# Kernel optimization log

Measured on AMD Instinct MI355X. Metric: run time of the kernel, lower is better.

The kernel has to match this reference:

```python
import jax, jax.numpy as jnp
import numpy as np

B, C, T = 8, 512, 2048
G = 32          # GroupNorm groups
HEADS = 8       # C // head_channels(64)
EPS = 1e-5


def setup_inputs() -> dict:
    key = jax.random.key(0)
    ks = jax.random.split(key, 7)
    s = 0.02
    return {
        "x": jax.random.normal(ks[0], (B, C, T), dtype=jnp.float32),
        "gn_w": jnp.ones((C,), dtype=jnp.float32),
        "gn_b": jnp.zeros((C,), dtype=jnp.float32),
        "qkv_w": jax.random.normal(ks[1], (3 * C, C), dtype=jnp.float32) * s,
        "qkv_b": jnp.zeros((3 * C,), dtype=jnp.float32),
        "proj_w": jax.random.normal(ks[2], (C, C), dtype=jnp.float32) * s,
        "proj_b": jnp.zeros((C,), dtype=jnp.float32),
    }


def reference(x, gn_w, gn_b, qkv_w, qkv_b, proj_w, proj_b):
    b, c, t = x.shape
    ch = c // HEADS
    # GroupNorm(32, C): normalize over (channels-in-group, T)
    xg = x.reshape(b, G, (c // G) * t)
    mu = jnp.mean(xg, axis=-1, keepdims=True)
    var = jnp.var(xg, axis=-1, keepdims=True)
    h = ((xg - mu) * jax.lax.rsqrt(var + EPS)).reshape(b, c, t)
    h = h * gn_w[:, None] + gn_b[:, None]
    # 1x1 Conv1d -> pointwise linear over channels
    qkv = jnp.einsum('oc,bct->bot', qkv_w, h) + qkv_b[:, None]  # [b, 3c, t]
    q, k, v = jnp.split(qkv, 3, axis=1)
    scale = ch ** -0.25
    q = (q * scale).reshape(b * HEADS, ch, t)
    k = (k * scale).reshape(b * HEADS, ch, t)
    v = v.reshape(b * HEADS, ch, t)
    w = jnp.einsum('bct,bcs->bts', q, k)  # [b*H, t, t]
    w = jax.nn.softmax(w.astype(jnp.float32), axis=-1).astype(q.dtype)
    a = jnp.einsum('bts,bcs->bct', w, v).reshape(b, c, t)
    out = jnp.einsum('oc,bct->bot', proj_w, a) + proj_b[:, None]
    return x + out
```

## Files before the change

### kernel.cpp

```cpp
#include <hip/hip_runtime.h>
#include <hip/hip_bf16.h>
#include <math.h>

#define NB 8
#define NC 512
#define NT 2048
#define NG 32
#define NH 8
#define CH 64

typedef __attribute__((ext_vector_type(8))) short short8;
typedef __attribute__((ext_vector_type(4))) short short4v;
typedef __attribute__((ext_vector_type(4))) float floatx4;
typedef __attribute__((ext_vector_type(2))) unsigned int uintx2;
typedef __attribute__((ext_vector_type(4))) unsigned int uintx4;

static __device__ __forceinline__ short f2bf(float f) {
    __hip_bfloat16 h = __float2bfloat16(f);
    return *reinterpret_cast<short*>(&h);
}

static __device__ __forceinline__ int pk2bf_trunc(float lo, float hi) {
    return (int)__builtin_amdgcn_perm(__builtin_bit_cast(unsigned, hi),
                                      __builtin_bit_cast(unsigned, lo),
                                      0x07060302u);
}

static __device__ __forceinline__ void gload_lds16(const short* g, short* l) {
    __builtin_amdgcn_global_load_lds(
        (const __attribute__((address_space(1))) void*)g,
        (__attribute__((address_space(3))) void*)l, 16, 0, 0);
}

__global__ __launch_bounds__(256) void castw_kernel(
    const float* __restrict__ qw, const float* __restrict__ pw,
    short* __restrict__ qo, short* __restrict__ po)
{
    const int i = blockIdx.x * 256 + threadIdx.x;
    const bool isq = i < 196608;
    const int j = isq ? i : i - 196608;
    float4 v = isq ? ((const float4*)qw)[j] : ((const float4*)pw)[j];
    short4v s;
    s.x = f2bf(v.x); s.y = f2bf(v.y); s.z = f2bf(v.z); s.w = f2bf(v.w);
    if (isq) *(short4v*)&qo[j * 4] = s;
    else     *(short4v*)&po[j * 4] = s;
}

__global__ __launch_bounds__(256) void gn_fused_kernel(
    const float* __restrict__ x, const float* __restrict__ gw,
    const float* __restrict__ gb, short* __restrict__ ht)
{
    __shared__ float xs[16 * NT];
    __shared__ float red[16];
    const int tid = threadIdx.x;
    const int wv = tid >> 6, lane = tid & 63;
    const int f = blockIdx.x;
    const int b = f & 7, g = f >> 3;

    const float* src = x + ((size_t)b * NC + g * 16) * NT;

    #pragma unroll
    for (int i = 0; i < 32; ++i) {
        const int slot = i * 256 + tid;
        gload_lds16((const short*)src + (size_t)slot * 8,
                    (short*)&xs[(i * 256 + wv * 64) * 4]);
    }
    __syncthreads();

    float s = 0.f, ss = 0.f;
    #pragma unroll
    for (int i = 0; i < 32; ++i) {
        float4 v = ((const float4*)xs)[i * 256 + tid];
        s  += v.x + v.y + v.z + v.w;
        ss += v.x*v.x + v.y*v.y + v.z*v.z + v.w*v.w;
    }
    #pragma unroll
    for (int o = 32; o > 0; o >>= 1) {
        s  += __shfl_down(s,  o, 64);
        ss += __shfl_down(ss, o, 64);
    }
    if (lane == 0) { red[wv] = s; red[8 + wv] = ss; }
    __syncthreads();
    const float inv  = 1.f / 32768.f;
    const float mean = (red[0] + red[1] + red[2] + red[3]) * inv;
    const float var  = (red[8] + red[9] + red[10] + red[11]) * inv - mean * mean;
    const float rstd = rsqrtf(var + 1e-5f);

    float wc[16], bc[16];
    #pragma unroll
    for (int ch = 0; ch < 16; ++ch) {
        const float w = gw[g * 16 + ch] * rstd;
        wc[ch] = w;
        bc[ch] = gb[g * 16 + ch] - mean * w;
    }

    #pragma unroll
    for (int k = 0; k < 2; ++k) {
        const int q = k * 256 + tid;
        float4 col[16];
        #pragma unroll
        for (int ch = 0; ch < 16; ++ch)
            col[ch] = *(const float4*)&xs[ch * NT + q * 4];
        short* dst = ht + ((size_t)b * NT + q * 4) * NC + g * 16;
        #pragma unroll
        for (int j = 0; j < 4; ++j) {
            short v16[16];
            #pragma unroll
            for (int ch = 0; ch < 16; ++ch) {
                const float xv = (j == 0) ? col[ch].x : (j == 1) ? col[ch].y
                               : (j == 2) ? col[ch].z : col[ch].w;
                v16[ch] = f2bf(xv * wc[ch] + bc[ch]);
            }
            *(short8*)&dst[(size_t)j * NC]     = *(const short8*)&v16[0];
            *(short8*)&dst[(size_t)j * NC + 8] = *(const short8*)&v16[8];
        }
    }
}

#define BK 32
__global__ __launch_bounds__(256) void qkv_gemm_kernel(
    const short* __restrict__ wb, const short* __restrict__ ht,
    const float* __restrict__ bias,
    short* __restrict__ q_t, short* __restrict__ k_t, short* __restrict__ vv)
{
    __shared__ short As[128 * BK];
    __shared__ short Bs[128 * BK];
    const int tid = threadIdx.x;
    const int wv = tid >> 6, lane = tid & 63;
    const int l16 = lane & 15, quad = lane >> 4;
    const int fblk = blockIdx.y * 128 + blockIdx.x;
    const int jx = fblk >> 3, xcd = fblk & 7;
    const int n0 = (xcd * 16 + jx / 12) * 128;
    const int m0 = (jx % 12) * 128;
    const int wm = wv & 1, wn = wv >> 1;

    floatx4 acc[4][4];
    #pragma unroll
    for (int i = 0; i < 4; ++i)
        #pragma unroll
        for (int j = 0; j < 4; ++j) acc[i][j] = (floatx4){0.f, 0.f, 0.f, 0.f};

    const short* gsrc = (wv < 2) ? wb : ht;
    const int rbase = (wv & 1) * 64;
    const int tile0 = (wv < 2) ? m0 : n0;
    short* lbuf = (wv < 2) ? As : Bs;
    const int lrow = lane >> 2;
    const int lcol = (lane & 3) * 8;

    for (int k0 = 0; k0 < 512; k0 += BK) {
        __syncthreads();
        #pragma unroll
        for (int ch = 0; ch < 4; ++ch) {
            const int row = rbase + ch * 16 + lrow;
            gload_lds16(gsrc + (size_t)(tile0 + row) * 512 + k0 + lcol,
                        lbuf + (rbase + ch * 16) * BK);
        }
        __syncthreads();

        short8 af[4], bfr[4];
        #pragma unroll
        for (int i = 0; i < 4; ++i) {
            af[i]  = *(const short8*)&As[(wm * 64 + i * 16 + l16) * BK + quad * 8];
            bfr[i] = *(const short8*)&Bs[(wn * 64 + i * 16 + l16) * BK + quad * 8];
        }
        #pragma unroll
        for (int i = 0; i < 4; ++i)
            #pragma unroll
            for (int j = 0; j < 4; ++j)
                acc[i][j] = __builtin_amdgcn_mfma_f32_16x16x32_bf16(
                    af[i], bfr[j], acc[i][j], 0, 0, 0);
    }

    const float kscale = 0.35355339059327373f;
    const float qscale = 0.35355339059327373f * 1.4426950408889634f;
    #pragma unroll
    for (int i = 0; i < 4; ++i) {
        const int o16 = m0 + wm * 64 + i * 16;
        const int sel = o16 >> 9;
        const int hh  = (o16 >> 6) & 7;
        const int c16 = o16 & 63;
        const float4 b4 = *(const float4*)&bias[o16 + quad * 4];
        const float sc = (sel == 0) ? qscale : kscale;
        #pragma unroll
        for (int j = 0; j < 4; ++j) {
            const int tg = n0 + wn * 64 + j * 16 + l16;
            const int b = tg >> 11, t = tg & 2047;
            floatx4 v = acc[i][j];
            v[0] += b4.x; v[1] += b4.y; v[2] += b4.z; v[3] += b4.w;
            if (sel < 2) {
                short4v s;
                s.x = f2bf(v[0] * sc); s.y = f2bf(v[1] * sc);
                s.z = f2bf(v[2] * sc); s.w = f2bf(v[3] * sc);
                short* dst = (sel == 0 ? q_t : k_t) +
                    (((size_t)(b * NH + hh) * NT + t) * CH + c16 + quad * 4);
                *(short4v*)dst = s;
            } else {
                short* dst = vv + ((size_t)(b * NH + hh) * CH + c16 + quad * 4) * NT + t;
                #pragma unroll
                for (int r = 0; r < 4; ++r) dst[(size_t)r * NT] = f2bf(v[r]);
            }
        }
    }
}

__global__ __launch_bounds__(512, 4) void attn_kernel(
    const short* __restrict__ qg, const short* __restrict__ kg,
    const short* __restrict__ vg, short* __restrict__ at)
{
    __shared__ short kt[2][64 * 64];
    __shared__ short vs[2][64 * 64];

    const int tid = threadIdx.x;
    const int wv = tid >> 6, lane = tid & 63;
    const int l16 = lane & 15, quad = lane >> 4;
    const int xr = l16 & 7;
    const int f = blockIdx.y * 8 + blockIdx.x;
    const int t0 = (f >> 6) * 256;
    const int bh = ((f >> 3) & 7) * 8 + (f & 7);
    const int b = bh >> 3, hd = bh & 7;
    const short* qh = qg + (size_t)bh * NT * CH;
    const short* kh = kg + (size_t)bh * NT * CH;
    const short* vh = vg + (size_t)bh * CH * NT;

    {
        const int row = tid >> 3, cc = (tid & 7) ^ (row & 7);
        gload_lds16(kh + (size_t)row * CH + cc * 8, &kt[0][wv * 512]);
        gload_lds16(vh + (size_t)row * NT + cc * 8, &vs[0][wv * 512]);
    }

    short8 bq[2][2];
    #pragma unroll
    for (int qt = 0; qt < 2; ++qt) {
        const int row = t0 + wv * 32 + qt * 16 + l16;
        #pragma unroll
        for (int ks = 0; ks < 2; ++ks)
            bq[qt][ks] = *(const short8*)&qh[(size_t)row * CH + ks * 32 + quad * 8];
    }
    __syncthreads();

    floatx4 Oa[4][2];
    #pragma unroll
    for (int ct = 0; ct < 4; ++ct)
        #pragma unroll
        for (int qt = 0; qt < 2; ++qt) Oa[ct][qt] = (floatx4){0.f, 0.f, 0.f, 0.f};
    float l_part[2] = {0.f, 0.f};

    for (int it = 0; it < NT / 64; ++it) {
        __syncthreads();
        if (it + 1 < NT / 64) {
            const int s0n = (it + 1) * 64;
            const int row = tid >> 3, cc = (tid & 7) ^ (row & 7);
            gload_lds16(kh + (size_t)(s0n + row) * CH + cc * 8,
                        &kt[(it + 1) & 1][wv * 512]);
            gload_lds16(vh + (size_t)row * NT + s0n + cc * 8,
                        &vs[(it + 1) & 1][wv * 512]);
        }
        const short* kc = kt[it & 1];
        const short* vc = vs[it & 1];

        floatx4 sacc[4][2];
        #pragma unroll
        for (int nt = 0; nt < 4; ++nt)
            #pragma unroll
            for (int qt = 0; qt < 2; ++qt) sacc[nt][qt] = (floatx4){0.f, 0.f, 0.f, 0.f};
        __builtin_amdgcn_s_setprio(1);
        #pragma unroll
        for (int ks = 0; ks < 2; ++ks) {
            const int c = (quad | (ks << 2)) ^ xr;
            #pragma unroll
            for (int nt = 0; nt < 4; ++nt) {
                short8 ak = *(const short8*)&kc[(nt * 16 + l16) * 64 + c * 8];
                #pragma unroll
                for (int qt = 0; qt < 2; ++qt)
                    sacc[nt][qt] = __builtin_amdgcn_mfma_f32_16x16x32_bf16(
                        ak, bq[qt][ks], sacc[nt][qt], 0, 0, 0);
            }
        }
        __builtin_amdgcn_s_setprio(0);

        unsigned pk01[2][4], pk23[2][4];
        #pragma unroll
        for (int qt = 0; qt < 2; ++qt) {
            float sn[4];
            #pragma unroll
            for (int nt = 0; nt < 4; ++nt) {
                const float p0 = __builtin_amdgcn_exp2f(sacc[nt][qt][0]);
                const float p1 = __builtin_amdgcn_exp2f(sacc[nt][qt][1]);
                const float p2 = __builtin_amdgcn_exp2f(sacc[nt][qt][2]);
                const float p3 = __builtin_amdgcn_exp2f(sacc[nt][qt][3]);
                sn[nt] = (p0 + p1) + (p2 + p3);
                pk01[qt][nt] = (unsigned)pk2bf_trunc(p0, p1);
                pk23[qt][nt] = (unsigned)pk2bf_trunc(p2, p3);
            }
            l_part[qt] += (sn[0] + sn[1]) + (sn[2] + sn[3]);
        }

        #pragma unroll
        for (int ks = 0; ks < 2; ++ks) {
            short8 bp[2];
            #pragma unroll
            for (int qt = 0; qt < 2; ++qt) {
                uintx2 a = __builtin_amdgcn_permlane32_swap(
                    pk01[qt][2 * ks], pk01[qt][2 * ks + 1], false, false);
                uintx2 w02 = __builtin_amdgcn_permlane16_swap(a.x, a.y, false, false);
                uintx2 c2 = __builtin_amdgcn_permlane32_swap(
                    pk23[qt][2 * ks], pk23[qt][2 * ks + 1], false, false);
                uintx2 w13 = __builtin_amdgcn_permlane16_swap(c2.x, c2.y, false, false);
                uintx4 wi = (uintx4){w02.x, w13.x, w02.y, w13.y};
                bp[qt] = __builtin_bit_cast(short8, wi);
            }
            const int c = (quad | (ks << 2)) ^ xr;
            __builtin_amdgcn_s_setprio(1);
            #pragma unroll
            for (int ct = 0; ct < 4; ++ct) {
                short8 av = *(const short8*)&vc[(ct * 16 + l16) * 64 + c * 8];
                #pragma unroll
                for (int qt = 0; qt < 2; ++qt)
                    Oa[ct][qt] = __builtin_amdgcn_mfma_f32_16x16x32_bf16(
                        av, bp[qt], Oa[ct][qt], 0, 0, 0);
            }
            __builtin_amdgcn_s_setprio(0);
        }
    }

    #pragma unroll
    for (int qt = 0; qt < 2; ++qt) {
        float l = l_part[qt];
        l += __shfl_xor(l, 16, 64);
        l += __shfl_xor(l, 32, 64);
        const float rl = 1.f / l;
        const int t = t0 + wv * 32 + qt * 16 + l16;
        short* dst = at + ((size_t)b * NT + t) * NC + hd * CH;
        #pragma unroll
        for (int ct = 0; ct < 4; ++ct) {
            int2 s;
            s.x = pk2bf_trunc(Oa[ct][qt][0] * rl, Oa[ct][qt][1] * rl);
            s.y = pk2bf_trunc(Oa[ct][qt][2] * rl, Oa[ct][qt][3] * rl);
            *(int2*)&dst[ct * 16 + quad * 4] = s;
        }
    }
}

__global__ __launch_bounds__(256) void proj_gemm_kernel(
    const short* __restrict__ wb, const short* __restrict__ at,
    const float* __restrict__ bias, const float* __restrict__ xres,
    float* __restrict__ out)
{
    __shared__ short As[128 * BK];
    __shared__ short Bs[128 * BK];
    const int tid = threadIdx.x;
    const int wv = tid >> 6, lane = tid & 63;
    const int l16 = lane & 15, quad = lane >> 4;
    const int fblk = blockIdx.y * 128 + blockIdx.x;
    const int jx = fblk >> 3, xcd = fblk & 7;
    const int n0 = (xcd * 16 + (jx >> 2)) * 128;
    const int m0 = (jx & 3) * 128;
    const int wm = wv & 1, wn = wv >> 1;

    floatx4 acc[4][4];
    #pragma unroll
    for (int i = 0; i < 4; ++i)
        #pragma unroll
        for (int j = 0; j < 4; ++j) acc[i][j] = (floatx4){0.f, 0.f, 0.f, 0.f};

    const short* gsrc = (wv < 2) ? wb : at;
    const int rbase = (wv & 1) * 64;
    const int tile0 = (wv < 2) ? m0 : n0;
    short* lbuf = (wv < 2) ? As : Bs;
    const int lrow = lane >> 2;
    const int lcol = (lane & 3) * 8;

    for (int k0 = 0; k0 < 512; k0 += BK) {
        __syncthreads();
        #pragma unroll
        for (int ch = 0; ch < 4; ++ch) {
            const int row = rbase + ch * 16 + lrow;
            gload_lds16(gsrc + (size_t)(tile0 + row) * 512 + k0 + lcol,
                        lbuf + (rbase + ch * 16) * BK);
        }
        __syncthreads();

        short8 af[4], bfr[4];
        #pragma unroll
        for (int i = 0; i < 4; ++i) {
            af[i]  = *(const short8*)&As[(wm * 64 + i * 16 + l16) * BK + quad * 8];
            bfr[i] = *(const short8*)&Bs[(wn * 64 + i * 16 + l16) * BK + quad * 8];
        }
        #pragma unroll
        for (int i = 0; i < 4; ++i)
            #pragma unroll
            for (int j = 0; j < 4; ++j)
                acc[i][j] = __builtin_amdgcn_mfma_f32_16x16x32_bf16(
                    af[i], bfr[j], acc[i][j], 0, 0, 0);
    }

    #pragma unroll
    for (int i = 0; i < 4; ++i) {
        const int o16 = m0 + wm * 64 + i * 16;
        const float4 b4 = *(const float4*)&bias[o16 + quad * 4];
        #pragma unroll
        for (int j = 0; j < 4; ++j) {
            const int tg = n0 + wn * 64 + j * 16 + l16;
            const int b = tg >> 11, t = tg & 2047;
            const size_t base = ((size_t)b * NC + o16 + quad * 4) * NT + t;
            floatx4 v = acc[i][j];
            out[base]          = v[0] + b4.x + xres[base];
            out[base + NT]     = v[1] + b4.y + xres[base + NT];
            out[base + 2 * NT] = v[2] + b4.z + xres[base + 2 * NT];
            out[base + 3 * NT] = v[3] + b4.w + xres[base + 3 * NT];
        }
    }
}

extern "C" void kernel_launch(void* const* d_in, const int* in_sizes, int n_in,
                              void* d_out, int out_size, void* d_ws, size_t ws_size,
                              hipStream_t stream)
{
    const float* x      = (const float*)d_in[0];
    const float* gn_w   = (const float*)d_in[1];
    const float* gn_b   = (const float*)d_in[2];
    const float* qkv_w  = (const float*)d_in[3];
    const float* qkv_b  = (const float*)d_in[4];
    const float* proj_w = (const float*)d_in[5];
    const float* proj_b = (const float*)d_in[6];
    float* out = (float*)d_out;

    short* ht  = (short*)d_ws;
    short* q_t = ht  + 8388608;
    short* k_t = q_t + 8388608;
    short* vv  = k_t + 8388608;
    short* at  = vv  + 8388608;
    short* qwb = at  + 8388608;
    short* pwb = qwb + 786432;

    castw_kernel<<<1024, 256, 0, stream>>>(qkv_w, proj_w, qwb, pwb);
    gn_fused_kernel<<<NB * NG, 256, 0, stream>>>(x, gn_w, gn_b, ht);
    qkv_gemm_kernel<<<dim3(128, 12), 256, 0, stream>>>(qwb, ht, qkv_b, q_t, k_t, vv);
    attn_kernel<<<dim3(NT / 256, NB * NH), 512, 0, stream>>>(q_t, k_t, vv, at);
    proj_gemm_kernel<<<dim3(128, 4), 256, 0, stream>>>(pwb, at, proj_b, x, out);
}
```

Before: 229.8 us.

## Halve attention query tile per block and widen GroupNorm blocks to 512 threads

The attention kernel now gives each wave 16 query rows instead of 32, so each block covers 128 queries and the grid doubles to 1024 blocks. Launch bounds are raised to 8 blocks per SM to boost occupancy and latency hiding. The cost is that every K/V tile is loaded from global memory and LDS twice as often per query, which lowers MFMA reuse. GroupNorm moves to 512 threads per block, with each thread doing one column pass instead of two, and the reduction now sums over 8 waves.

```diff
diff --git a/kernel.cpp b/kernel.cpp
--- a/kernel.cpp
+++ b/kernel.cpp
@@ -46,7 +46,7 @@
     else     *(short4v*)&po[j * 4] = s;
 }
 
-__global__ __launch_bounds__(256) void gn_fused_kernel(
+__global__ __launch_bounds__(512) void gn_fused_kernel(
     const float* __restrict__ x, const float* __restrict__ gw,
     const float* __restrict__ gb, short* __restrict__ ht)
 {
@@ -60,17 +60,17 @@
     const float* src = x + ((size_t)b * NC + g * 16) * NT;
 
     #pragma unroll
-    for (int i = 0; i < 32; ++i) {
-        const int slot = i * 256 + tid;
+    for (int i = 0; i < 16; ++i) {
+        const int slot = i * 512 + tid;
         gload_lds16((const short*)src + (size_t)slot * 8,
-                    (short*)&xs[(i * 256 + wv * 64) * 4]);
+                    (short*)&xs[(i * 512 + wv * 64) * 4]);
     }
     __syncthreads();
 
     float s = 0.f, ss = 0.f;
     #pragma unroll
-    for (int i = 0; i < 32; ++i) {
-        float4 v = ((const float4*)xs)[i * 256 + tid];
+    for (int i = 0; i < 16; ++i) {
+        float4 v = ((const float4*)xs)[i * 512 + tid];
         s  += v.x + v.y + v.z + v.w;
         ss += v.x*v.x + v.y*v.y + v.z*v.z + v.w*v.w;
     }
@@ -82,8 +82,11 @@
     if (lane == 0) { red[wv] = s; red[8 + wv] = ss; }
     __syncthreads();
     const float inv  = 1.f / 32768.f;
-    const float mean = (red[0] + red[1] + red[2] + red[3]) * inv;
-    const float var  = (red[8] + red[9] + red[10] + red[11]) * inv - mean * mean;
+    const float mean = (((red[0] + red[1]) + (red[2] + red[3])) +
+                        ((red[4] + red[5]) + (red[6] + red[7]))) * inv;
+    const float var  = (((red[8] + red[9]) + (red[10] + red[11])) +
+                        ((red[12] + red[13]) + (red[14] + red[15]))) * inv
+                       - mean * mean;
     const float rstd = rsqrtf(var + 1e-5f);
 
     float wc[16], bc[16];
@@ -94,9 +97,8 @@
         bc[ch] = gb[g * 16 + ch] - mean * w;
     }
 
-    #pragma unroll
-    for (int k = 0; k < 2; ++k) {
-        const int q = k * 256 + tid;
+    {
+        const int q = tid;
         float4 col[16];
         #pragma unroll
         for (int ch = 0; ch < 16; ++ch)
@@ -203,7 +205,7 @@
     }
 }
 
-__global__ __launch_bounds__(512, 4) void attn_kernel(
+__global__ __launch_bounds__(512, 8) void attn_kernel(
     const short* __restrict__ qg, const short* __restrict__ kg,
     const short* __restrict__ vg, short* __restrict__ at)
 {
@@ -214,8 +216,8 @@
     const int wv = tid >> 6, lane = tid & 63;
     const int l16 = lane & 15, quad = lane >> 4;
     const int xr = l16 & 7;
-    const int f = blockIdx.y * 8 + blockIdx.x;
-    const int t0 = (f >> 6) * 256;
+    const int f = blockIdx.y * 16 + blockIdx.x;
+    const int t0 = (f >> 6) * 128;
     const int bh = ((f >> 3) & 7) * 8 + (f & 7);
     const int b = bh >> 3, hd = bh & 7;
     const short* qh = qg + (size_t)bh * NT * CH;
@@ -228,22 +230,19 @@
         gload_lds16(vh + (size_t)row * NT + cc * 8, &vs[0][wv * 512]);
     }
 
-    short8 bq[2][2];
-    #pragma unroll
-    for (int qt = 0; qt < 2; ++qt) {
-        const int row = t0 + wv * 32 + qt * 16 + l16;
+    short8 bq[2];
+    {
+        const int row = t0 + wv * 16 + l16;
         #pragma unroll
         for (int ks = 0; ks < 2; ++ks)
-            bq[qt][ks] = *(const short8*)&qh[(size_t)row * CH + ks * 32 + quad * 8];
+            bq[ks] = *(const short8*)&qh[(size_t)row * CH + ks * 32 + quad * 8];
     }
     __syncthreads();
 
-    floatx4 Oa[4][2];
-    #pragma unroll
-    for (int ct = 0; ct < 4; ++ct)
-        #pragma unroll
-        for (int qt = 0; qt < 2; ++qt) Oa[ct][qt] = (floatx4){0.f, 0.f, 0.f, 0.f};
-    float l_part[2] = {0.f, 0.f};
+    floatx4 Oa[4];
+    #pragma unroll
+    for (int ct = 0; ct < 4; ++ct) Oa[ct] = (floatx4){0.f, 0.f, 0.f, 0.f};
+    float l_part = 0.f;
 
     for (int it = 0; it < NT / 64; ++it) {
         __syncthreads();
@@ -258,11 +257,9 @@
         const short* kc = kt[it & 1];
         const short* vc = vs[it & 1];
 
-        floatx4 sacc[4][2];
-        #pragma unroll
-        for (int nt = 0; nt < 4; ++nt)
-            #pragma unroll
-            for (int qt = 0; qt < 2; ++qt) sacc[nt][qt] = (floatx4){0.f, 0.f, 0.f, 0.f};
+        floatx4 sacc[4];
+        #pragma unroll
+        for (int nt = 0; nt < 4; ++nt) sacc[nt] = (floatx4){0.f, 0.f, 0.f, 0.f};
         __builtin_amdgcn_s_setprio(1);
         #pragma unroll
         for (int ks = 0; ks < 2; ++ks) {
@@ -270,72 +267,65 @@
             #pragma unroll
             for (int nt = 0; nt < 4; ++nt) {
                 short8 ak = *(const short8*)&kc[(nt * 16 + l16) * 64 + c * 8];
-                #pragma unroll
-                for (int qt = 0; qt < 2; ++qt)
-                    sacc[nt][qt] = __builtin_amdgcn_mfma_f32_16x16x32_bf16(
-                        ak, bq[qt][ks], sacc[nt][qt], 0, 0, 0);
+                sacc[nt] = __builtin_amdgcn_mfma_f32_16x16x32_bf16(
+                    ak, bq[ks], sacc[nt], 0, 0, 0);
             }
         }
         __builtin_amdgcn_s_setprio(0);
 
-        unsigned pk01[2][4], pk23[2][4];
-        #pragma unroll
-        for (int qt = 0; qt < 2; ++qt) {
+        unsigned pk01[4], pk23[4];
+        {
             float sn[4];
             #pragma unroll
             for (int nt = 0; nt < 4; ++nt) {
-                const float p0 = __builtin_amdgcn_exp2f(sacc[nt][qt][0]);
-                const float p1 = __builtin_amdgcn_exp2f(sacc[nt][qt][1]);
-                const float p2 = __builtin_amdgcn_exp2f(sacc[nt][qt][2]);
-                const float p3 = __builtin_amdgcn_exp2f(sacc[nt][qt][3]);
+                const float p0 = __builtin_amdgcn_exp2f(sacc[nt][0]);
+                const float p1 = __builtin_amdgcn_exp2f(sacc[nt][1]);
+                const float p2 = __builtin_amdgcn_exp2f(sacc[nt][2]);
+                const float p3 = __builtin_amdgcn_exp2f(sacc[nt][3]);
                 sn[nt] = (p0 + p1) + (p2 + p3);
-                pk01[qt][nt] = (unsigned)pk2bf_trunc(p0, p1);
-                pk23[qt][nt] = (unsigned)pk2bf_trunc(p2, p3);
-            }
-            l_part[qt] += (sn[0] + sn[1]) + (sn[2] + sn[3]);
+                pk01[nt] = (unsigned)pk2bf_trunc(p0, p1);
+                pk23[nt] = (unsigned)pk2bf_trunc(p2, p3);
+            }
+            l_part += (sn[0] + sn[1]) + (sn[2] + sn[3]);
         }
 
         #pragma unroll
         for (int ks = 0; ks < 2; ++ks) {
-            short8 bp[2];
-            #pragma unroll
-            for (int qt = 0; qt < 2; ++qt) {
+            short8 bp;
+            {
                 uintx2 a = __builtin_amdgcn_permlane32_swap(
-                    pk01[qt][2 * ks], pk01[qt][2 * ks + 1], false, false);
+                    pk01[2 * ks], pk01[2 * ks + 1], false, false);
                 uintx2 w02 = __builtin_amdgcn_permlane16_swap(a.x, a.y, false, false);
                 uintx2 c2 = __builtin_amdgcn_permlane32_swap(
-                    pk23[qt][2 * ks], pk23[qt][2 * ks + 1], false, false);
+                    pk23[2 * ks], pk23[2 * ks + 1], false, false);
                 uintx2 w13 = __builtin_amdgcn_permlane16_swap(c2.x, c2.y, false, false);
                 uintx4 wi = (uintx4){w02.x, w13.x, w02.y, w13.y};
-                bp[qt] = __builtin_bit_cast(short8, wi);
+                bp = __builtin_bit_cast(short8, wi);
             }
             const int c = (quad | (ks << 2)) ^ xr;
             __builtin_amdgcn_s_setprio(1);
             #pragma unroll
             for (int ct = 0; ct < 4; ++ct) {
                 short8 av = *(const short8*)&vc[(ct * 16 + l16) * 64 + c * 8];
-                #pragma unroll
-                for (int qt = 0; qt < 2; ++qt)
-                    Oa[ct][qt] = __builtin_amdgcn_mfma_f32_16x16x32_bf16(
-                        av, bp[qt], Oa[ct][qt], 0, 0, 0);
+                Oa[ct] = __builtin_amdgcn_mfma_f32_16x16x32_bf16(
+                    av, bp, Oa[ct], 0, 0, 0);
             }
             __builtin_amdgcn_s_setprio(0);
         }
     }
 
-    #pragma unroll
-    for (int qt = 0; qt < 2; ++qt) {
-        float l = l_part[qt];
+    {
+        float l = l_part;
         l += __shfl_xor(l, 16, 64);
         l += __shfl_xor(l, 32, 64);
         const float rl = 1.f / l;
-        const int t = t0 + wv * 32 + qt * 16 + l16;
+        const int t = t0 + wv * 16 + l16;
         short* dst = at + ((size_t)b * NT + t) * NC + hd * CH;
         #pragma unroll
         for (int ct = 0; ct < 4; ++ct) {
             int2 s;
-            s.x = pk2bf_trunc(Oa[ct][qt][0] * rl, Oa[ct][qt][1] * rl);
-            s.y = pk2bf_trunc(Oa[ct][qt][2] * rl, Oa[ct][qt][3] * rl);
+            s.x = pk2bf_trunc(Oa[ct][0] * rl, Oa[ct][1] * rl);
+            s.y = pk2bf_trunc(Oa[ct][2] * rl, Oa[ct][3] * rl);
             *(int2*)&dst[ct * 16 + quad * 4] = s;
         }
     }
@@ -434,8 +424,8 @@
     short* pwb = qwb + 786432;
 
     castw_kernel<<<1024, 256, 0, stream>>>(qkv_w, proj_w, qwb, pwb);
-    gn_fused_kernel<<<NB * NG, 256, 0, stream>>>(x, gn_w, gn_b, ht);
+    gn_fused_kernel<<<NB * NG, 512, 0, stream>>>(x, gn_w, gn_b, ht);
     qkv_gemm_kernel<<<dim3(128, 12), 256, 0, stream>>>(qwb, ht, qkv_b, q_t, k_t, vv);
-    attn_kernel<<<dim3(NT / 256, NB * NH), 512, 0, stream>>>(q_t, k_t, vv, at);
+    attn_kernel<<<dim3(16, 64), 512, 0, stream>>>(q_t, k_t, vv, at);
     proj_gemm_kernel<<<dim3(128, 4), 256, 0, stream>>>(pwb, at, proj_b, x, out);
 }
```

Result: slower. 242.2 us (+5.4%).
